# Kernel tuning notes

Measured on AMD Instinct MI355X. Metric: run time of the kernel, lower is better.

## Reference

```python
import jax, jax.numpy as jnp
import numpy as np

S, D, H = 4096, 1024, 16
DK = D // H
LN_EPS = 1e-5


def setup_inputs() -> dict:
    key = jax.random.key(0)
    ks = jax.random.split(key, 7)
    sc = 1.0 / np.sqrt(DK)
    x = jax.random.normal(ks[0], (S, D), dtype=jnp.float32)
    Wq = jax.random.normal(ks[1], (H, DK, DK), dtype=jnp.float32) * sc
    Wk = jax.random.normal(ks[2], (H, DK, DK), dtype=jnp.float32) * sc
    Wv = jax.random.normal(ks[3], (H, DK, DK), dtype=jnp.float32) * sc
    bq = jax.random.normal(ks[4], (H, DK), dtype=jnp.float32) * 0.02
    bk = jax.random.normal(ks[5], (H, DK), dtype=jnp.float32) * 0.02
    bv = jax.random.normal(ks[6], (H, DK), dtype=jnp.float32) * 0.02
    gamma = jnp.ones((D,), dtype=jnp.float32)
    beta = jnp.zeros((D,), dtype=jnp.float32)
    return {"x": x, "Wq": Wq, "bq": bq, "Wk": Wk, "bk": bk,
            "Wv": Wv, "bv": bv, "gamma": gamma, "beta": beta}


def reference(x, Wq, bq, Wk, bk, Wv, bv, gamma, beta):
    s, d = x.shape
    h, dk, _ = Wq.shape
    xh = x.reshape(s, h, dk)  # per-head slice of x
    # torch Linear: y = x @ W.T + b  -> einsum 'shd,hed->she'
    q = jnp.einsum('shd,hed->she', xh, Wq) + bq
    k = jnp.einsum('shd,hed->she', xh, Wk) + bk
    v = jnp.einsum('shd,hed->she', xh, Wv) + bv
    scale = 1.0 / jnp.sqrt(jnp.asarray(dk, x.dtype))
    scores = jnp.einsum('she,the->hst', q, k) * scale  # [H,S,S]
    attn = jax.nn.softmax(scores, axis=-1)
    o = jnp.einsum('hst,the->she', attn, v)  # [S,H,dk]
    A = o.reshape(s, d)  # concat heads
    # dropout is identity in eval mode
    mu = jnp.mean(A, axis=-1, keepdims=True)
    var = jnp.var(A, axis=-1, keepdims=True)
    An = (A - mu) * jax.lax.rsqrt(var + LN_EPS) * gamma + beta
    return x + An
```

## Files before the change

### kernel.cpp

```cpp
#include <hip/hip_runtime.h>
#include <math.h>
#include <stdint.h>

#define S_LEN 4096
#define NH 16
#define TILES 64

typedef __attribute__((ext_vector_type(4))) float f32x4;
typedef __attribute__((ext_vector_type(8))) short sh8;
typedef __attribute__((ext_vector_type(4))) short sh4;
typedef _Float16 half_t;

__device__ __forceinline__ void mfma_first(f32x4& d, sh8 a, sh8 b) {
  asm("s_nop 1\n\tv_mfma_f32_16x16x32_f16 %0, %1, %2, %0" : "+v"(d) : "v"(a), "v"(b));
}
__device__ __forceinline__ void mfma_last(f32x4& d, sh8 a, sh8 b) {
  asm("v_mfma_f32_16x16x32_f16 %0, %1, %2, %0\n\ts_nop 7\n\ts_nop 1" : "+v"(d) : "v"(a), "v"(b));
}
__device__ __forceinline__ void mfma_v(f32x4& d, sh8 a, sh8 b) {
  asm("s_nop 2\n\tv_mfma_f32_16x16x32_f16 %0, %1, %2, %0" : "+v"(d) : "v"(a), "v"(b));
}
__device__ __forceinline__ void mfma_vlast(f32x4& d, sh8 a, sh8 b) {
  asm("s_nop 2\n\tv_mfma_f32_16x16x32_f16 %0, %1, %2, %0\n\ts_nop 7\n\ts_nop 1" : "+v"(d) : "v"(a), "v"(b));
}

__device__ __forceinline__ short h_bits(half_t h) {
  union { half_t h; short s; } u; u.h = h; return u.s;
}

__global__ __launch_bounds__(256) void qkv_proj(
    const float* __restrict__ x,
    const float* __restrict__ Wq, const float* __restrict__ bq,
    const float* __restrict__ Wk, const float* __restrict__ bk,
    const float* __restrict__ Wv, const float* __restrict__ bv,
    half_t* __restrict__ Qg, half_t* __restrict__ Kg, half_t* __restrict__ VTg)
{
  const int h = blockIdx.y;
  const int s0 = blockIdx.x << 6;
  const int tid = threadIdx.x, wv = tid >> 6, lane = tid & 63;
  const int g = lane >> 4, ln = lane & 15;

  sh8 ax[2];
  const float* xrow = x + ((size_t)(s0 + (wv << 4) + ln) << 10) + (h << 6);
#pragma unroll
  for (int sl = 0; sl < 2; ++sl) {
    const f32x4 x0 = *(const f32x4*)(xrow + (sl << 5) + (g << 3));
    const f32x4 x1 = *(const f32x4*)(xrow + (sl << 5) + (g << 3) + 4);
#pragma unroll
    for (int j = 0; j < 4; ++j) {
      ax[sl][j]     = h_bits((half_t)x0[j]);
      ax[sl][4 + j] = h_bits((half_t)x1[j]);
    }
  }

#pragma unroll
  for (int mat = 0; mat < 3; ++mat) {
    const float* Wsrc = (mat == 0) ? Wq : (mat == 1) ? Wk : Wv;
    const float* bsrc = (mat == 0) ? bq : (mat == 1) ? bk : bv;

    f32x4 acc[4];
#pragma unroll
    for (int ct = 0; ct < 4; ++ct) acc[ct] = (f32x4){0.f, 0.f, 0.f, 0.f};

#pragma unroll
    for (int ct = 0; ct < 4; ++ct) {
      const float* wrow = Wsrc + (h << 12) + (((ct << 4) + ln) << 6);
#pragma unroll
      for (int sl = 0; sl < 2; ++sl) {
        const f32x4 w0 = *(const f32x4*)(wrow + (sl << 5) + (g << 3));
        const f32x4 w1 = *(const f32x4*)(wrow + (sl << 5) + (g << 3) + 4);
        sh8 bw;
#pragma unroll
        for (int j = 0; j < 4; ++j) {
          bw[j]     = h_bits((half_t)w0[j]);
          bw[4 + j] = h_bits((half_t)w1[j]);
        }
        if (ct == 3 && sl == 1) mfma_vlast(acc[ct], ax[sl], bw);
        else                    mfma_v(acc[ct], ax[sl], bw);
      }
    }

    const float scl = (mat == 0) ? 0.125f * 1.44269504f : 1.0f;
    if (mat < 2) {
      half_t* plane = (mat == 0) ? Qg : Kg;
#pragma unroll
      for (int ct = 0; ct < 4; ++ct) {
        const float be = bsrc[(h << 6) + (ct << 4) + ln];
#pragma unroll
        for (int r = 0; r < 4; ++r) {
          const int srow = s0 + (wv << 4) + (g << 2) + r;
          plane[(((size_t)h * S_LEN + srow) << 6) + (ct << 4) + ln] =
              (half_t)((acc[ct][r] + be) * scl);
        }
      }
    } else {
#pragma unroll
      for (int ct = 0; ct < 4; ++ct) {
        const float be = bsrc[(h << 6) + (ct << 4) + ln];
        sh4 pk;
#pragma unroll
        for (int r = 0; r < 4; ++r) pk[r] = h_bits((half_t)(acc[ct][r] + be));
        half_t* dst = VTg + ((((size_t)h * 64 + blockIdx.x) << 6) + (ct << 4) + ln) * 64
                      + (wv << 4) + (g << 2);
        *(sh4*)dst = pk;
      }
    }
  }
}

__global__ __launch_bounds__(256, 4) void attn_fa(
    const half_t* __restrict__ Qg, const half_t* __restrict__ Kg,
    const half_t* __restrict__ VTg, float* __restrict__ og)
{
  const int b = blockIdx.x;
  const int h = ((b & 7) << 1) | ((b >> 3) & 1);
  const int s0 = (b >> 4) << 6;
  const int tid = threadIdx.x, wv = tid >> 6, lane = tid & 63;
  const int g = lane >> 4, ln = lane & 15;

  __shared__ half_t KB[2][2][64][64];
  __shared__ half_t P[4][16][64];
  char* Pw = (char*)&P[wv][0][0];

  const int qrow = s0 + (wv << 4) + ln;
  const half_t* qb = Qg + (((size_t)h * S_LEN + qrow) << 6);
  const sh8 aq0 = *(const sh8*)(qb + (g << 3));
  const sh8 aq1 = *(const sh8*)(qb + 32 + (g << 3));

  const int srcswz = ((lane >> 3) << 7) | (((lane & 7) ^ (lane >> 3)) << 4);
  const int p0 = (g ^ (ln & 15 & 7)) << 4;

  const char* srcK = (const char*)Kg + ((size_t)h << 19);
  const char* srcV = (const char*)VTg + ((size_t)h << 19);

  auto STAGE = [&](int buf, int t) {
    const size_t toff = (size_t)t << 13;
#pragma unroll
    for (int i = 0; i < 2; ++i) {
      const int row0 = (wv << 4) + (i << 3);
      const int rb = row0 << 7;
      __builtin_amdgcn_global_load_lds((const uint32_t*)(srcK + toff + rb + srcswz),
                                       (uint32_t*)&KB[buf][0][row0][0], 16, 0, 0);
      __builtin_amdgcn_global_load_lds((const uint32_t*)(srcV + toff + rb + srcswz),
                                       (uint32_t*)&KB[buf][1][row0][0], 16, 0, 0);
    }
  };

  f32x4 oacc[4];
#pragma unroll
  for (int nt = 0; nt < 4; ++nt) oacc[nt] = (f32x4){0.f, 0.f, 0.f, 0.f};
  float l_part[4] = {0.f, 0.f, 0.f, 0.f};

  STAGE(0, 0);
  __syncthreads();

  int cur = 0;
  for (int t = 0; t < TILES; ++t) {
    if (t + 1 < TILES) STAGE(cur ^ 1, t + 1);

    const char* kb_base = (const char*)&KB[cur][0][0][0];
    f32x4 sc[4];
    __builtin_amdgcn_s_setprio(1);
#pragma unroll
    for (int ct = 0; ct < 4; ++ct) {
      const int a0 = (((ct << 4) + ln) << 7) + p0;
      const sh8 kh0 = *(const sh8*)(kb_base + a0);
      const sh8 kh1 = *(const sh8*)(kb_base + (a0 ^ 64));
      f32x4 d = (f32x4){0.f, 0.f, 0.f, 0.f};
      mfma_first(d, aq0, kh0);
      mfma_last(d, aq1, kh1);
      sc[ct] = d;
    }
    __builtin_amdgcn_s_setprio(0);

#pragma unroll
    for (int ct = 0; ct < 4; ++ct) {
#pragma unroll
      for (int r = 0; r < 4; ++r) {
        const float p = exp2f(sc[ct][r]);
        l_part[r] += p;
        const int row = (g << 2) + r;
        const int off = (row << 7) + (((((ct << 1) + (ln >> 3)) ^ (row & 7)) << 4))
                        + ((ln & 7) << 1);
        *(half_t*)(Pw + off) = (half_t)p;
      }
    }
    const int pr0 = (ln << 7) + ((g ^ (ln & 7)) << 4);
    const sh8 pa0 = *(const sh8*)(Pw + pr0);
    const sh8 pa1 = *(const sh8*)(Pw + (pr0 ^ 64));

    const char* vb_base = (const char*)&KB[cur][1][0][0];
    __builtin_amdgcn_s_setprio(1);
#pragma unroll
    for (int nt = 0; nt < 4; ++nt) {
      const int a0 = (((nt << 4) + ln) << 7) + p0;
      const sh8 vb0 = *(const sh8*)(vb_base + a0);
      const sh8 vb1 = *(const sh8*)(vb_base + (a0 ^ 64));
      f32x4 d = oacc[nt];
      mfma_first(d, pa0, vb0);
      mfma_last(d, pa1, vb1);
      oacc[nt] = d;
    }
    __builtin_amdgcn_s_setprio(0);

    __syncthreads();
    cur ^= 1;
  }

#pragma unroll
  for (int r = 0; r < 4; ++r) {
    float lt = l_part[r];
    lt += __shfl_xor(lt, 1);
    lt += __shfl_xor(lt, 2);
    lt += __shfl_xor(lt, 4);
    lt += __shfl_xor(lt, 8);
    const float inv = 1.0f / lt;
    const int row = s0 + (wv << 4) + (g << 2) + r;
#pragma unroll
    for (int nt = 0; nt < 4; ++nt)
      og[(((size_t)row * NH + h) << 6) + (nt << 4) + ln] = oacc[nt][r] * inv;
  }
}

__global__ __launch_bounds__(256) void ln_res(
    const float* __restrict__ x, const float* __restrict__ o,
    const float* __restrict__ gamma, const float* __restrict__ beta,
    float* __restrict__ out)
{
  const int s = blockIdx.x;
  const int tid = threadIdx.x;
  const size_t base = ((size_t)s << 10) + (tid << 2);
  const f32x4 a = *(const f32x4*)(o + base);
  float sm = a[0] + a[1] + a[2] + a[3];
  float sq = a[0]*a[0] + a[1]*a[1] + a[2]*a[2] + a[3]*a[3];
#pragma unroll
  for (int off = 1; off < 64; off <<= 1) {
    sm += __shfl_xor(sm, off);
    sq += __shfl_xor(sq, off);
  }
  __shared__ float redc[2][4];
  if ((tid & 63) == 0) { redc[0][tid >> 6] = sm; redc[1][tid >> 6] = sq; }
  __syncthreads();
  sm = redc[0][0] + redc[0][1] + redc[0][2] + redc[0][3];
  sq = redc[1][0] + redc[1][1] + redc[1][2] + redc[1][3];
  const float mu = sm * (1.f / 1024.f);
  const float var = sq * (1.f / 1024.f) - mu * mu;
  const float rs = rsqrtf(var + 1e-5f);
  const f32x4 xv = *(const f32x4*)(x + base);
  const f32x4 gv = *(const f32x4*)(gamma + (tid << 2));
  const f32x4 bv = *(const f32x4*)(beta + (tid << 2));
  f32x4 r;
#pragma unroll
  for (int j = 0; j < 4; ++j) r[j] = xv[j] + (a[j] - mu) * rs * gv[j] + bv[j];
  *(f32x4*)(out + base) = r;
}

extern "C" void kernel_launch(void* const* d_in, const int* in_sizes, int n_in,
                              void* d_out, int out_size, void* d_ws, size_t ws_size,
                              hipStream_t stream) {
  const float* x     = (const float*)d_in[0];
  const float* Wq    = (const float*)d_in[1];
  const float* bq    = (const float*)d_in[2];
  const float* Wk    = (const float*)d_in[3];
  const float* bk    = (const float*)d_in[4];
  const float* Wv    = (const float*)d_in[5];
  const float* bv    = (const float*)d_in[6];
  const float* gamma = (const float*)d_in[7];
  const float* beta  = (const float*)d_in[8];
  float* out = (float*)d_out;

  const size_t pe = (size_t)S_LEN * NH * 64;
  if (ws_size < 40u * 1024u * 1024u) return;
  half_t* Qg  = (half_t*)d_ws;
  half_t* Kg  = Qg + pe;
  half_t* VTg = Kg + pe;
  float*  o   = (float*)(VTg + pe);

  qkv_proj<<<dim3(64, 16), 256, 0, stream>>>(x, Wq, bq, Wk, bk, Wv, bv, Qg, Kg, VTg);
  attn_fa<<<dim3(1024), 256, 0, stream>>>(Qg, Kg, VTg, o);
  ln_res<<<dim3(4096), 256, 0, stream>>>(x, o, gamma, beta, out);
}
```

Baseline: 244.6 us.

## Compute transposed scores so P stays in registers and double query rows per wave

```diff
diff --git a/kernel.cpp b/kernel.cpp
--- a/kernel.cpp
+++ b/kernel.cpp
@@ -10,22 +10,39 @@
 typedef __attribute__((ext_vector_type(8))) short sh8;
 typedef __attribute__((ext_vector_type(4))) short sh4;
 typedef _Float16 half_t;
-
-__device__ __forceinline__ void mfma_first(f32x4& d, sh8 a, sh8 b) {
-  asm("s_nop 1\n\tv_mfma_f32_16x16x32_f16 %0, %1, %2, %0" : "+v"(d) : "v"(a), "v"(b));
-}
-__device__ __forceinline__ void mfma_last(f32x4& d, sh8 a, sh8 b) {
-  asm("v_mfma_f32_16x16x32_f16 %0, %1, %2, %0\n\ts_nop 7\n\ts_nop 1" : "+v"(d) : "v"(a), "v"(b));
-}
+typedef __attribute__((ext_vector_type(8))) _Float16 h8;
+typedef __attribute__((ext_vector_type(4))) _Float16 h4;
+typedef __attribute__((ext_vector_type(2))) __fp16 fp16x2;
+
 __device__ __forceinline__ void mfma_v(f32x4& d, sh8 a, sh8 b) {
   asm("s_nop 2\n\tv_mfma_f32_16x16x32_f16 %0, %1, %2, %0" : "+v"(d) : "v"(a), "v"(b));
 }
 __device__ __forceinline__ void mfma_vlast(f32x4& d, sh8 a, sh8 b) {
   asm("s_nop 2\n\tv_mfma_f32_16x16x32_f16 %0, %1, %2, %0\n\ts_nop 7\n\ts_nop 1" : "+v"(d) : "v"(a), "v"(b));
 }
+__device__ __forceinline__ void mfma32_init(f32x4& d, h8 a, h8 b, f32x4 z) {
+  asm("v_mfma_f32_16x16x32_f16 %0, %1, %2, %3" : "=&v"(d) : "v"(a), "v"(b), "v"(z));
+}
+__device__ __forceinline__ void mfma32_acc(f32x4& d, h8 a, h8 b) {
+  asm("v_mfma_f32_16x16x32_f16 %0, %1, %2, %0" : "+v"(d) : "v"(a), "v"(b));
+}
+__device__ __forceinline__ void mfma32_acc_last(f32x4& d, h8 a, h8 b) {
+  asm("v_mfma_f32_16x16x32_f16 %0, %1, %2, %0\n\ts_nop 7\n\ts_nop 1" : "+v"(d) : "v"(a), "v"(b));
+}
+__device__ __forceinline__ void mfma16_acc(f32x4& d, h4 a, h4 b) {
+  asm("v_mfma_f32_16x16x16_f16 %0, %1, %2, %0" : "+v"(d) : "v"(a), "v"(b));
+}
+__device__ __forceinline__ void mfma16_first(f32x4& d, h4 a, h4 b) {
+  asm("s_nop 2\n\tv_mfma_f32_16x16x16_f16 %0, %1, %2, %0" : "+v"(d) : "v"(a), "v"(b));
+}
 
 __device__ __forceinline__ short h_bits(half_t h) {
   union { half_t h; short s; } u; u.h = h; return u.s;
+}
+__device__ __forceinline__ h4 pack_h4(fp16x2 lo, fp16x2 hi) {
+  union { fp16x2 v[2]; h4 h; } u;
+  u.v[0] = lo; u.v[1] = hi;
+  return u.h;
 }
 
 __global__ __launch_bounds__(256) void qkv_proj(
@@ -101,37 +118,49 @@
 #pragma unroll
         for (int r = 0; r < 4; ++r) pk[r] = h_bits((half_t)(acc[ct][r] + be));
         half_t* dst = VTg + ((((size_t)h * 64 + blockIdx.x) << 6) + (ct << 4) + ln) * 64
-                      + (wv << 4) + (g << 2);
+                      + (g << 4) + (wv << 2);
         *(sh4*)dst = pk;
       }
     }
   }
 }
 
-__global__ __launch_bounds__(256, 4) void attn_fa(
+__global__ __launch_bounds__(256, 2) void attn_fa(
     const half_t* __restrict__ Qg, const half_t* __restrict__ Kg,
     const half_t* __restrict__ VTg, float* __restrict__ og)
 {
   const int b = blockIdx.x;
   const int h = ((b & 7) << 1) | ((b >> 3) & 1);
-  const int s0 = (b >> 4) << 6;
+  const int s0 = (b >> 4) << 7;
   const int tid = threadIdx.x, wv = tid >> 6, lane = tid & 63;
   const int g = lane >> 4, ln = lane & 15;
 
   __shared__ half_t KB[2][2][64][64];
-  __shared__ half_t P[4][16][64];
-  char* Pw = (char*)&P[wv][0][0];
-
-  const int qrow = s0 + (wv << 4) + ln;
-  const half_t* qb = Qg + (((size_t)h * S_LEN + qrow) << 6);
-  const sh8 aq0 = *(const sh8*)(qb + (g << 3));
-  const sh8 aq1 = *(const sh8*)(qb + 32 + (g << 3));
+
+  h8 aq[2][2];
+#pragma unroll
+  for (int a = 0; a < 2; ++a) {
+    const int qrow = s0 + (wv << 5) + (a << 4) + ln;
+    const half_t* qb = Qg + (((size_t)h * S_LEN + qrow) << 6);
+    aq[a][0] = *(const h8*)(qb + (g << 3));
+    aq[a][1] = *(const h8*)(qb + 32 + (g << 3));
+  }
 
   const int srcswz = ((lane >> 3) << 7) | (((lane & 7) ^ (lane >> 3)) << 4);
-  const int p0 = (g ^ (ln & 15 & 7)) << 4;
+  int ka[4], kax[4];
+#pragma unroll
+  for (int ct = 0; ct < 4; ++ct) {
+    ka[ct]  = (((ct << 4) + ln) << 7) + ((g ^ (ln & 7)) << 4);
+    kax[ct] = ka[ct] ^ 64;
+  }
+  int va[2];
+#pragma unroll
+  for (int p = 0; p < 2; ++p)
+    va[p] = (ln << 7) + ((((g << 1) + p) ^ (ln & 7)) << 4);
 
   const char* srcK = (const char*)Kg + ((size_t)h << 19);
   const char* srcV = (const char*)VTg + ((size_t)h << 19);
+  const char* ldsb = (const char*)&KB[0][0][0][0];
 
   auto STAGE = [&](int buf, int t) {
     const size_t toff = (size_t)t << 13;
@@ -146,79 +175,98 @@
     }
   };
 
-  f32x4 oacc[4];
-#pragma unroll
-  for (int nt = 0; nt < 4; ++nt) oacc[nt] = (f32x4){0.f, 0.f, 0.f, 0.f};
-  float l_part[4] = {0.f, 0.f, 0.f, 0.f};
+  f32x4 oacc[2][4];
+#pragma unroll
+  for (int a = 0; a < 2; ++a)
+#pragma unroll
+    for (int nt = 0; nt < 4; ++nt) oacc[a][nt] = (f32x4){0.f, 0.f, 0.f, 0.f};
+  float l_part[2] = {0.f, 0.f};
+  const f32x4 zc = (f32x4){0.f, 0.f, 0.f, 0.f};
 
   STAGE(0, 0);
   __syncthreads();
 
-  int cur = 0;
-  for (int t = 0; t < TILES; ++t) {
-    if (t + 1 < TILES) STAGE(cur ^ 1, t + 1);
-
-    const char* kb_base = (const char*)&KB[cur][0][0][0];
-    f32x4 sc[4];
-    __builtin_amdgcn_s_setprio(1);
-#pragma unroll
-    for (int ct = 0; ct < 4; ++ct) {
-      const int a0 = (((ct << 4) + ln) << 7) + p0;
-      const sh8 kh0 = *(const sh8*)(kb_base + a0);
-      const sh8 kh1 = *(const sh8*)(kb_base + (a0 ^ 64));
-      f32x4 d = (f32x4){0.f, 0.f, 0.f, 0.f};
-      mfma_first(d, aq0, kh0);
-      mfma_last(d, aq1, kh1);
-      sc[ct] = d;
-    }
-    __builtin_amdgcn_s_setprio(0);
-
-#pragma unroll
-    for (int ct = 0; ct < 4; ++ct) {
-#pragma unroll
-      for (int r = 0; r < 4; ++r) {
-        const float p = exp2f(sc[ct][r]);
-        l_part[r] += p;
-        const int row = (g << 2) + r;
-        const int off = (row << 7) + (((((ct << 1) + (ln >> 3)) ^ (row & 7)) << 4))
-                        + ((ln & 7) << 1);
-        *(half_t*)(Pw + off) = (half_t)p;
+  for (int t = 0; t < TILES; t += 2) {
+#pragma unroll
+    for (int pass = 0; pass < 2; ++pass) {
+      const int u = t + pass;
+      constexpr int BUFS = 16384, VOFF = 8192;
+      const int buf = pass;
+      if (u + 1 < TILES) STAGE(buf ^ 1, u + 1);
+
+      h8 kb[4][2], vb[4][2];
+#pragma unroll
+      for (int ct = 0; ct < 4; ++ct) {
+        kb[ct][0] = *(const h8*)(ldsb + buf * BUFS + ka[ct]);
+        kb[ct][1] = *(const h8*)(ldsb + buf * BUFS + kax[ct]);
       }
-    }
-    const int pr0 = (ln << 7) + ((g ^ (ln & 7)) << 4);
-    const sh8 pa0 = *(const sh8*)(Pw + pr0);
-    const sh8 pa1 = *(const sh8*)(Pw + (pr0 ^ 64));
-
-    const char* vb_base = (const char*)&KB[cur][1][0][0];
-    __builtin_amdgcn_s_setprio(1);
-#pragma unroll
-    for (int nt = 0; nt < 4; ++nt) {
-      const int a0 = (((nt << 4) + ln) << 7) + p0;
-      const sh8 vb0 = *(const sh8*)(vb_base + a0);
-      const sh8 vb1 = *(const sh8*)(vb_base + (a0 ^ 64));
-      f32x4 d = oacc[nt];
-      mfma_first(d, pa0, vb0);
-      mfma_last(d, pa1, vb1);
-      oacc[nt] = d;
-    }
-    __builtin_amdgcn_s_setprio(0);
-
-    __syncthreads();
-    cur ^= 1;
-  }
-
-#pragma unroll
-  for (int r = 0; r < 4; ++r) {
-    float lt = l_part[r];
-    lt += __shfl_xor(lt, 1);
-    lt += __shfl_xor(lt, 2);
-    lt += __shfl_xor(lt, 4);
-    lt += __shfl_xor(lt, 8);
+#pragma unroll
+      for (int nt = 0; nt < 4; ++nt)
+#pragma unroll
+        for (int p = 0; p < 2; ++p)
+          vb[nt][p] = *(const h8*)(ldsb + buf * BUFS + VOFF + (nt << 11) + va[p]);
+
+      f32x4 sc[2][4];
+      __builtin_amdgcn_s_setprio(1);
+#pragma unroll
+      for (int a = 0; a < 2; ++a)
+#pragma unroll
+        for (int ct = 0; ct < 4; ++ct) {
+          mfma32_init(sc[a][ct], kb[ct][0], aq[a][0], zc);
+          if (a == 1 && ct == 3) mfma32_acc_last(sc[a][ct], kb[ct][1], aq[a][1]);
+          else                   mfma32_acc(sc[a][ct], kb[ct][1], aq[a][1]);
+        }
+      __builtin_amdgcn_s_setprio(0);
+      __builtin_amdgcn_sched_barrier(0);
+
+      h4 pa[2][4];
+#pragma unroll
+      for (int a = 0; a < 2; ++a)
+#pragma unroll
+        for (int ct = 0; ct < 4; ++ct) {
+          const float e0 = exp2f(sc[a][ct][0]);
+          const float e1 = exp2f(sc[a][ct][1]);
+          const float e2 = exp2f(sc[a][ct][2]);
+          const float e3 = exp2f(sc[a][ct][3]);
+          l_part[a] += (e0 + e1) + (e2 + e3);
+          pa[a][ct] = pack_h4(__builtin_amdgcn_cvt_pkrtz(e0, e1),
+                              __builtin_amdgcn_cvt_pkrtz(e2, e3));
+        }
+      __builtin_amdgcn_sched_barrier(0);
+
+      __builtin_amdgcn_s_setprio(1);
+#pragma unroll
+      for (int a = 0; a < 2; ++a)
+#pragma unroll
+        for (int nt = 0; nt < 4; ++nt)
+#pragma unroll
+          for (int ct = 0; ct < 4; ++ct) {
+            const h4 vf = (ct & 1)
+              ? __builtin_shufflevector(vb[nt][ct >> 1], vb[nt][ct >> 1], 4, 5, 6, 7)
+              : __builtin_shufflevector(vb[nt][ct >> 1], vb[nt][ct >> 1], 0, 1, 2, 3);
+            if (a == 0 && nt == 0 && ct == 0) mfma16_first(oacc[a][nt], pa[a][ct], vf);
+            else                              mfma16_acc(oacc[a][nt], pa[a][ct], vf);
+          }
+      __builtin_amdgcn_s_setprio(0);
+
+      __syncthreads();
+    }
+  }
+
+#pragma unroll
+  for (int a = 0; a < 2; ++a) {
+    float lt = l_part[a];
+    lt += __shfl_xor(lt, 16);
+    lt += __shfl_xor(lt, 32);
     const float inv = 1.0f / lt;
-    const int row = s0 + (wv << 4) + (g << 2) + r;
-#pragma unroll
-    for (int nt = 0; nt < 4; ++nt)
-      og[(((size_t)row * NH + h) << 6) + (nt << 4) + ln] = oacc[nt][r] * inv;
+#pragma unroll
+    for (int r = 0; r < 4; ++r) {
+      const float linv = __shfl(inv, (g << 2) + r);
+      const int row = s0 + (wv << 5) + (a << 4) + (g << 2) + r;
+#pragma unroll
+      for (int nt = 0; nt < 4; ++nt)
+        og[(((size_t)row * NH + h) << 6) + (nt << 4) + ln] = oacc[a][nt][r] * linv;
+    }
   }
 }
 
@@ -277,6 +325,6 @@
   float*  o   = (float*)(VTg + pe);
 
   qkv_proj<<<dim3(64, 16), 256, 0, stream>>>(x, Wq, bq, Wk, bk, Wv, bv, Qg, Kg, VTg);
-  attn_fa<<<dim3(1024), 256, 0, stream>>>(Qg, Kg, VTg, o);
+  attn_fa<<<dim3(512), 256, 0, stream>>>(Qg, Kg, VTg, o);
   ln_res<<<dim3(4096), 256, 0, stream>>>(x, o, gamma, beta, out);
 }
```

Result: faster. 225.5 us (-7.8%).
